# Kernel tuning notes

Measured on AMD Instinct MI355X. Metric: run time of the kernel, lower is better.

Reference implementation:

```python
import jax, jax.numpy as jnp
import numpy as np

N_NODES = 10000
N_EDGES = 160000
MUL = 128            # channel multiplicity of node features
N_ELEM = 10          # node_attrs scalars (num elements)
N_EDGE_FEATS = 8     # radial basis size
W_NUMEL = 4 * MUL    # 4 uvu paths, 128 weights each
AVG_NEIGH = 16.0
INV_SQRT3 = 0.5773502691896258  # CG coefficient for 1o x 1o -> 0e (dot product path)


def setup_inputs() -> dict:
    key = jax.random.key(0)
    ks = jax.random.split(key, 12)
    node_attrs = jax.random.uniform(ks[0], (N_NODES, N_ELEM), dtype=jnp.float32)
    node_feats = jax.random.normal(ks[1], (N_NODES, MUL * 4), dtype=jnp.float32)  # 128x0e + 128x1o flattened
    edge_attrs = jax.random.normal(ks[2], (N_EDGES, 4), dtype=jnp.float32)        # Y0 (1) + Y1 (3)
    edge_feats = jax.random.normal(ks[3], (N_EDGES, N_EDGE_FEATS), dtype=jnp.float32)
    edge_index = jax.random.randint(ks[4], (2, N_EDGES), 0, N_NODES, dtype=jnp.int64)
    # learned parameters (xavier-ish scales; e3nn path norms folded into weights)
    W_up0 = jax.random.normal(ks[5], (MUL, MUL), dtype=jnp.float32) / np.sqrt(MUL)
    W_up1 = jax.random.normal(ks[6], (MUL, MUL), dtype=jnp.float32) / np.sqrt(MUL)
    W_tpw = jax.random.normal(ks[7], (N_ELEM, N_EDGE_FEATS, W_NUMEL), dtype=jnp.float32) / np.sqrt(N_ELEM * N_EDGE_FEATS)
    W_lin0 = jax.random.normal(ks[8], (2 * MUL, MUL), dtype=jnp.float32) / np.sqrt(2 * MUL)
    W_lin1 = jax.random.normal(ks[9], (2 * MUL, MUL), dtype=jnp.float32) / np.sqrt(2 * MUL)
    W_sk0 = jax.random.normal(ks[10], (MUL, N_ELEM, MUL), dtype=jnp.float32) / np.sqrt(MUL * N_ELEM)
    W_sk1 = jax.random.normal(ks[11], (MUL, N_ELEM, MUL), dtype=jnp.float32) / np.sqrt(MUL * N_ELEM)
    return dict(node_attrs=node_attrs, node_feats=node_feats, edge_attrs=edge_attrs,
                edge_feats=edge_feats, edge_index=edge_index,
                W_up0=W_up0, W_up1=W_up1, W_tpw=W_tpw,
                W_lin0=W_lin0, W_lin1=W_lin1, W_sk0=W_sk0, W_sk1=W_sk1)


def reference(node_attrs, node_feats, edge_attrs, edge_feats, edge_index,
              W_up0, W_up1, W_tpw, W_lin0, W_lin1, W_sk0, W_sk1):
    N = node_feats.shape[0]
    sender, receiver = edge_index[0], edge_index[1]
    x0 = node_feats[:, :MUL]                       # [N,128] scalars (0e)
    x1 = node_feats[:, MUL:].reshape(N, MUL, 3)    # [N,128,3] vectors (1o)

    # skip_tp: FullyConnectedTensorProduct(node_feats, node_attrs -> 128x0e+128x1o)
    sc0 = jnp.einsum('nu,na,uak->nk', x0, node_attrs, W_sk0)        # [N,128]
    sc1 = jnp.einsum('num,na,uak->nkm', x1, node_attrs, W_sk1)      # [N,128,3]

    # linear_up: per-l linear
    h0 = x0 @ W_up0                                   # [N,128]
    h1 = jnp.einsum('num,uk->nkm', x1, W_up1)         # [N,128,3]

    # per-edge TP weights: einsum('be,ba,aek->bk')
    tpw = jnp.einsum('be,ba,aek->bk', edge_feats, node_attrs[sender], W_tpw)  # [E,512]
    w1, w2, w3, w4 = tpw[:, :MUL], tpw[:, MUL:2*MUL], tpw[:, 2*MUL:3*MUL], tpw[:, 3*MUL:]

    Y0 = edge_attrs[:, 0]       # [E]
    Y1 = edge_attrs[:, 1:4]     # [E,3]
    hs0 = h0[sender]            # [E,128] gather
    hs1 = h1[sender]            # [E,128,3]

    # conv_tp (uvu, external per-edge weights), 4 CG paths:
    m0a = w1 * hs0 * Y0[:, None]                                       # 0e x 0e -> 0e
    m1a = (w2 * hs0)[:, :, None] * Y1[:, None, :]                      # 0e x 1o -> 1o
    m1b = hs1 * (w3 * Y0[:, None])[:, :, None]                         # 1o x 0e -> 1o
    m0b = w4 * (INV_SQRT3 * jnp.einsum('eum,em->eu', hs1, Y1))         # 1o x 1o -> 0e
    m0 = jnp.concatenate([m0a, m0b], axis=1)    # [E,256]  irreps_mid 0e block
    m1 = jnp.concatenate([m1a, m1b], axis=1)    # [E,256,3] irreps_mid 1o block

    # scatter_sum over receiver
    msg0 = jax.ops.segment_sum(m0, receiver, num_segments=N)   # [N,256]
    msg1 = jax.ops.segment_sum(m1, receiver, num_segments=N)   # [N,256,3]

    # linear (irreps_mid -> 128x0e+128x1o) / avg_num_neighbors + skip
    out0 = (msg0 @ W_lin0) / AVG_NEIGH + sc0                        # [N,128]
    out1 = jnp.einsum('num,uk->nkm', msg1, W_lin1) / AVG_NEIGH + sc1  # [N,128,3]
    return jnp.concatenate([out0, out1.reshape(N, MUL * 3)], axis=1)  # [N,512]
```

## Files before the change

### kernel.cpp

```cpp
#include <hip/hip_runtime.h>

#define NN 10000
#define NE 160000
#define NBK0 157
#define NBK1 469

constexpr float INV_AVG = 1.0f / 16.0f;
constexpr float INV_SQRT3F = 0.5773502691896258f;

typedef __attribute__((ext_vector_type(8))) short short8v;
typedef __attribute__((ext_vector_type(8))) unsigned short ushort8v;
typedef __attribute__((ext_vector_type(4))) float float4v;

#define OF_UP0 0
#define OF_UP1 16384
#define OF_SK0 32768
#define OF_SK1 196608
#define OF_LN0 360448
#define OF_LN1 393216
#define WPK_TOT 425984
#define WTP_TOT 49152

__device__ __forceinline__ unsigned short f2bf(float f) {
    unsigned int u = __float_as_uint(f);
    return (unsigned short)((u + 0x7FFFu + ((u >> 16) & 1u)) >> 16);
}
__device__ __forceinline__ float bf2f(unsigned short h) {
    return __uint_as_float(((unsigned int)h) << 16);
}

__global__ __launch_bounds__(256) void prep_w_kernel(
    const float* __restrict__ W_up0, const float* __restrict__ W_up1,
    const float* __restrict__ W_sk0, const float* __restrict__ W_sk1,
    const float* __restrict__ W_lin0, const float* __restrict__ W_lin1,
    unsigned short* __restrict__ wpk)
{
    const int g = blockIdx.x * 256 + threadIdx.x;
    if (g >= WPK_TOT / 8) return;
    const float* src; int local, base;
    if (g < 2048)       { src = W_up0;  local = g;         base = OF_UP0; }
    else if (g < 4096)  { src = W_up1;  local = g - 2048;  base = OF_UP1; }
    else if (g < 24576) { src = W_sk0;  local = g - 4096;  base = OF_SK0; }
    else if (g < 45056) { src = W_sk1;  local = g - 24576; base = OF_SK1; }
    else if (g < 49152) { src = W_lin0; local = g - 45056; base = OF_LN0; }
    else                { src = W_lin1; local = g - 49152; base = OF_LN1; }
    const int k8 = local >> 7, n = local & 127;
    ushort8v v;
    #pragma unroll
    for (int j = 0; j < 8; ++j)
        v[j] = f2bf(src[(size_t)(k8 * 8 + j) * 128 + n]);
    *(ushort8v*)(wpk + (size_t)base + (size_t)local * 8) = v;
}

__global__ __launch_bounds__(256) void prep_wt_kernel(
    const float* __restrict__ W_tpw, unsigned short* __restrict__ wtp)
{
    const int g = blockIdx.x * 256 + threadIdx.x;
    if (g >= 6144) return;
    const int k8 = g >> 9, col = g & 511;
    ushort8v v;
    #pragma unroll
    for (int j = 0; j < 8; ++j) {
        const int k = k8 * 8 + j;
        v[j] = (k < 80) ? f2bf(W_tpw[(size_t)k * 512 + col]) : (unsigned short)0;
    }
    *(ushort8v*)(wtp + (size_t)g * 8) = v;
}

__global__ __launch_bounds__(256, 2) void node_mfma_kernel(
    const float* __restrict__ node_attrs,
    const float* __restrict__ node_feats,
    const unsigned short* __restrict__ wpk,
    float* __restrict__ hbuf,
    float* __restrict__ out)
{
    __shared__ __align__(16) unsigned short habuf[1024][8];
    __shared__ __align__(16) unsigned short abuf[512][8];
    __shared__ __align__(16) unsigned short bbuf[1024][8];

    const int t = threadIdx.x;
    const int bid = blockIdx.x;
    const bool m1 = (bid >= NBK0);
    const int r0 = m1 ? (bid - NBK0) * 64 : bid * 64;
    const int RTOT = m1 ? 30000 : 10000;

    const unsigned short* __restrict__ wup = wpk + (m1 ? OF_UP1 : OF_UP0);
    const unsigned short* __restrict__ wsk = wpk + (m1 ? OF_SK1 : OF_SK0);

    const int rg_ = t >> 2, pg_ = t & 3;
    const int rr_g = min(r0 + rg_, RTOT - 1);
    int n_g, m_g;
    if (!m1) { n_g = rr_g; m_g = 0; }
    else     { n_g = rr_g / 3; m_g = rr_g - n_g * 3; }
    const int wq = rg_ >> 4, rlq = rg_ & 15;

    float atr[10];
    #pragma unroll
    for (int a = 0; a < 10; ++a) atr[a] = node_attrs[n_g * 10 + a];

    #pragma unroll
    for (int q = 0; q < 4; ++q) {
        const int sl = pg_ * 4 + q, ss = sl >> 2, kb = sl & 3;
        const int k0 = ss * 32 + kb * 8;
        ushort8v v;
        if (!m1) {
            const float4 xa_ = *(const float4*)(node_feats + (size_t)n_g * 512 + k0);
            const float4 xb_ = *(const float4*)(node_feats + (size_t)n_g * 512 + k0 + 4);
            v[0] = f2bf(xa_.x); v[1] = f2bf(xa_.y); v[2] = f2bf(xa_.z); v[3] = f2bf(xa_.w);
            v[4] = f2bf(xb_.x); v[5] = f2bf(xb_.y); v[6] = f2bf(xb_.z); v[7] = f2bf(xb_.w);
        } else {
            #pragma unroll
            for (int j = 0; j < 8; ++j)
                v[j] = f2bf(node_feats[(size_t)n_g * 512 + 128 + (k0 + j) * 3 + m_g]);
        }
        *(ushort8v*)&habuf[((ss * 4 + wq) * 4 + kb) * 16 + rlq][0] = v;
    }
    __syncthreads();

    const int w = t >> 6, lane = t & 63;
    const int rl = lane & 15, kq = lane >> 4;

    {
        float4v hacc[8];
        #pragma unroll
        for (int nt = 0; nt < 8; ++nt) hacc[nt] = (float4v){0.f, 0.f, 0.f, 0.f};

        #pragma unroll
        for (int ss = 0; ss < 4; ++ss) {
            const short8v af = *(const short8v*)&habuf[((ss * 4 + w) * 4 + kq) * 16 + rl][0];
            #pragma unroll
            for (int nt = 0; nt < 8; ++nt) {
                const short8v bf = *(const short8v*)(wup +
                    ((size_t)((ss * 4 + kq) * 128 + nt * 16 + rl)) * 8);
                hacc[nt] = __builtin_amdgcn_mfma_f32_16x16x32_bf16(af, bf, hacc[nt], 0, 0, 0);
            }
        }
        #pragma unroll
        for (int nt = 0; nt < 8; ++nt)
            #pragma unroll
            for (int v2 = 0; v2 < 4; ++v2) {
                const int rr = r0 + w * 16 + kq * 4 + v2;
                if (rr < RTOT) {
                    const int col = nt * 16 + rl;
                    if (!m1) hbuf[(size_t)rr * 512 + col] = hacc[nt][v2];
                    else {
                        const int n = rr / 3, m = rr - n * 3;
                        hbuf[(size_t)n * 512 + 128 + m * 128 + col] = hacc[nt][v2];
                    }
                }
            }
    }

    float4v sacc[8];
    #pragma unroll
    for (int nt = 0; nt < 8; ++nt) sacc[nt] = (float4v){0.f, 0.f, 0.f, 0.f};

    for (int ks = 0; ks < 20; ++ks) {
        __syncthreads();

        #pragma unroll
        for (int s2 = 0; s2 < 2; ++s2) {
            const int sl = pg_ * 2 + s2, ss = sl >> 2, kb = sl & 3;
            const int k0 = ks * 64 + ss * 32 + kb * 8;
            ushort8v v;
            #pragma unroll
            for (int j = 0; j < 8; ++j) {
                const int k = k0 + j;
                const int u = k / 10, a = k - u * 10;
                const unsigned short xh =
                    habuf[(((u >> 5) * 4 + wq) * 4 + ((u >> 3) & 3)) * 16 + rlq][u & 7];
                v[j] = f2bf(bf2f(xh) * atr[a]);
            }
            *(ushort8v*)&abuf[((ss * 4 + wq) * 4 + kb) * 16 + rlq][0] = v;
        }

        #pragma unroll
        for (int i = 0; i < 4; ++i) {
            const int s = i * 256 + t;
            const int ssb = s >> 9, ntb = (s >> 6) & 7, kbb = (s >> 4) & 3, nlb = s & 15;
            const int k8 = ks * 8 + ssb * 4 + kbb;
            const int n = ntb * 16 + nlb;
            *(ushort8v*)&bbuf[s][0] =
                *(const ushort8v*)(wsk + ((size_t)(k8 * 128 + n)) * 8);
        }
        __syncthreads();

        #pragma unroll
        for (int ss = 0; ss < 2; ++ss) {
            const short8v af = *(const short8v*)&abuf[((ss * 4 + w) * 4 + kq) * 16 + rl][0];
            #pragma unroll
            for (int nt = 0; nt < 8; ++nt) {
                const short8v bf = *(const short8v*)&bbuf[((ss * 8 + nt) * 4 + kq) * 16 + rl][0];
                sacc[nt] = __builtin_amdgcn_mfma_f32_16x16x32_bf16(af, bf, sacc[nt], 0, 0, 0);
            }
        }
    }

    #pragma unroll
    for (int nt = 0; nt < 8; ++nt)
        #pragma unroll
        for (int v2 = 0; v2 < 4; ++v2) {
            const int rr = r0 + w * 16 + kq * 4 + v2;
            if (rr < RTOT) {
                const int col = nt * 16 + rl;
                if (!m1) out[(size_t)rr * 512 + col] = sacc[nt][v2];
                else {
                    const int n = rr / 3, m = rr - n * 3;
                    out[(size_t)n * 512 + 128 + col * 3 + m] = sacc[nt][v2];
                }
            }
        }
}

__global__ __launch_bounds__(256) void hist_kernel(
    const int* __restrict__ recv, int* __restrict__ cnt)
{
    const int e = blockIdx.x * 256 + threadIdx.x;
    if (e < NE) atomicAdd(&cnt[recv[e]], 1);
}

__global__ __launch_bounds__(256) void scan_kernel(
    const int* __restrict__ cnt, int* __restrict__ row_start,
    int* __restrict__ head)
{
    __shared__ int part[256];
    const int t = threadIdx.x;
    const int base = t * 40;
    int s = 0;
    if (base < NN)
        for (int b = 0; b < 40; ++b) s += cnt[base + b];
    part[t] = s;
    __syncthreads();
    const int local = s;
    for (int off = 1; off < 256; off <<= 1) {
        const int v = (t >= off) ? part[t - off] : 0;
        __syncthreads();
        part[t] += v;
        __syncthreads();
    }
    const int excl = part[t] - local;
    if (base < NN) {
        int run = excl;
        for (int b = 0; b < 40; ++b) {
            row_start[base + b] = run;
            head[base + b] = run;
            run += cnt[base + b];
        }
    }
    if (t == 0) row_start[NN] = NE;
}

__global__ __launch_bounds__(256) void scatter_kernel(
    const int* __restrict__ recv, int* __restrict__ head,
    int* __restrict__ elist)
{
    const int e = blockIdx.x * 256 + threadIdx.x;
    if (e < NE) {
        const int p = atomicAdd(&head[recv[e]], 1);
        elist[p] = e;
    }
}

__global__ __launch_bounds__(256) void pack2_kernel(
    const float* __restrict__ node_attrs,
    const float* __restrict__ edge_attrs,
    const float* __restrict__ edge_feats,
    const int*  __restrict__ edge_index,
    const int*  __restrict__ elist,
    unsigned short* __restrict__ zpk,
    float* __restrict__ ypk)
{
    const int pos = blockIdx.x * 256 + threadIdx.x;
    if (pos >= NE) return;
    const int e = elist[pos];
    const int snd = edge_index[e];

    float ef[8];
    *(float4*)&ef[0] = *(const float4*)(edge_feats + (size_t)e * 8);
    *(float4*)&ef[4] = *(const float4*)(edge_feats + (size_t)e * 8 + 4);
    float at[10];
    #pragma unroll
    for (int a = 0; a < 10; ++a) at[a] = node_attrs[(size_t)snd * 10 + a];

    #pragma unroll
    for (int k8 = 0; k8 < 12; ++k8) {
        ushort8v v;
        #pragma unroll
        for (int j = 0; j < 8; ++j) {
            const int A = k8 * 8 + j;
            const float z = (A < 80) ? at[A >> 3] * ef[A & 7] : 0.f;
            v[j] = f2bf(z);
        }
        *(ushort8v*)(zpk + ((size_t)k8 * NE + pos) * 8) = v;
    }

    const float4 ea = *(const float4*)(edge_attrs + (size_t)e * 4);
    *(float4*)(ypk + (size_t)pos * 8) = ea;
    *(float4*)(ypk + (size_t)pos * 8 + 4) =
        make_float4(__int_as_float(snd), 0.f, 0.f, 0.f);
}

__global__ __launch_bounds__(256, 2) void gather_mfma_kernel(
    const unsigned short* __restrict__ wtp,
    const float* __restrict__ hbuf,
    const int*  __restrict__ row_start,
    const unsigned short* __restrict__ zpk,
    const float* __restrict__ ypk,
    float* __restrict__ msgbuf)
{
    __shared__ __align__(16) unsigned short zb[384][8];
    __shared__ float yb[32][9];

    const int t = threadIdx.x;
    const int p = blockIdx.x & 1;
    const int ngrp = blockIdx.x >> 1;
    const int w = t >> 6, lane = t & 63;
    const int rl = lane & 15, kq = lane >> 4;

    short8v breg[2][3][2];
    #pragma unroll
    for (int wi = 0; wi < 2; ++wi)
        #pragma unroll
        for (int ks = 0; ks < 3; ++ks)
            #pragma unroll
            for (int ct = 0; ct < 2; ++ct) {
                const int col = p * 256 + wi * 128 + w * 32 + ct * 16 + rl;
                breg[wi][ks][ct] = *(const short8v*)(wtp +
                    ((size_t)((ks * 4 + kq) * 512 + col)) * 8);
            }

    for (int nn = 0; nn < 4; ++nn) {
        const int node = ngrp * 4 + nn;
        const int rowst = row_start[node];
        const int deg = row_start[node + 1] - rowst;

        float nacc[2][4];
        #pragma unroll
        for (int ct = 0; ct < 2; ++ct)
            #pragma unroll
            for (int j = 0; j < 4; ++j) nacc[ct][j] = 0.f;

        for (int ce = 0; ce < deg; ce += 32) {
            const int cl = min(32, deg - ce);
            __syncthreads();

            {
                const int s = t;
                const int rl2 = s & 15, kq2 = (s >> 4) & 3;
                const int rowt2 = (s >> 6) & 1, ks2 = s >> 7;
                const int e = rowt2 * 16 + rl2;
                const int k8 = ks2 * 4 + kq2;
                ushort8v v = {0, 0, 0, 0, 0, 0, 0, 0};
                if (e < cl)
                    v = *(const ushort8v*)(zpk + ((size_t)k8 * NE + rowst + ce + e) * 8);
                *(ushort8v*)&zb[s][0] = v;
            }
            {
                const int s = 256 + t;
                if (s < 384) {
                    const int rl2 = s & 15, kq2 = (s >> 4) & 3;
                    const int rowt2 = (s >> 6) & 1, ks2 = s >> 7;
                    const int e = rowt2 * 16 + rl2;
                    const int k8 = ks2 * 4 + kq2;
                    ushort8v v = {0, 0, 0, 0, 0, 0, 0, 0};
                    if (e < cl)
                        v = *(const ushort8v*)(zpk + ((size_t)k8 * NE + rowst + ce + e) * 8);
                    *(ushort8v*)&zb[s][0] = v;
                }
            }
            if (t < 64) {
                const int row = t >> 1, half = t & 1;
                float4 v = make_float4(0.f, 0.f, 0.f, 0.f);
                if (row < cl)
                    v = *(const float4*)(ypk + (size_t)(rowst + ce + row) * 8 + half * 4);
                yb[row][half * 4 + 0] = v.x;
                yb[row][half * 4 + 1] = v.y;
                yb[row][half * 4 + 2] = v.z;
                yb[row][half * 4 + 3] = v.w;
            }
            __syncthreads();

            if (p == 0) {
                #pragma unroll
                for (int rt = 0; rt < 2; ++rt) {
                    if (rt == 1 && cl <= 16) continue;
                    float h0v[4][2];
                    #pragma unroll
                    for (int v = 0; v < 4; ++v) {
                        const int e = rt * 16 + kq * 4 + v;
                        const int snd = __float_as_int(yb[e][4]);
                        const float* hrow = hbuf + (size_t)snd * 512;
                        #pragma unroll
                        for (int ct = 0; ct < 2; ++ct)
                            h0v[v][ct] = hrow[w * 32 + ct * 16 + rl];
                    }
                    float4v acc[2][2];
                    #pragma unroll
                    for (int wi = 0; wi < 2; ++wi)
                        #pragma unroll
                        for (int ct = 0; ct < 2; ++ct)
                            acc[wi][ct] = (float4v){0.f, 0.f, 0.f, 0.f};
                    #pragma unroll
                    for (int ks = 0; ks < 3; ++ks) {
                        const short8v af =
                            *(const short8v*)&zb[ks * 128 + rt * 64 + lane][0];
                        #pragma unroll
                        for (int wi = 0; wi < 2; ++wi)
                            #pragma unroll
                            for (int ct = 0; ct < 2; ++ct)
                                acc[wi][ct] = __builtin_amdgcn_mfma_f32_16x16x32_bf16(
                                    af, breg[wi][ks][ct], acc[wi][ct], 0, 0, 0);
                    }
                    #pragma unroll
                    for (int v = 0; v < 4; ++v) {
                        const int e = rt * 16 + kq * 4 + v;
                        const float Y0  = yb[e][0];
                        const float Y10 = yb[e][1];
                        const float Y11 = yb[e][2];
                        const float Y12 = yb[e][3];
                        #pragma unroll
                        for (int ct = 0; ct < 2; ++ct) {
                            const float tA = acc[0][ct][v];
                            const float tB = acc[1][ct][v];
                            const float h0 = h0v[v][ct];
                            nacc[ct][0] = fmaf(tA * Y0, h0, nacc[ct][0]);
                            const float tm = tB * h0;
                            nacc[ct][1] = fmaf(tm, Y10, nacc[ct][1]);
                            nacc[ct][2] = fmaf(tm, Y11, nacc[ct][2]);
                            nacc[ct][3] = fmaf(tm, Y12, nacc[ct][3]);
                        }
                    }
                }
            } else {
                #pragma unroll
                for (int rt = 0; rt < 2; ++rt) {
                    if (rt == 1 && cl <= 16) continue;
                    float hA[4][2], hB[4][2], hC[4][2];
                    #pragma unroll
                    for (int v = 0; v < 4; ++v) {
                        const int e = rt * 16 + kq * 4 + v;
                        const int snd = __float_as_int(yb[e][4]);
                        const float* hrow = hbuf + (size_t)snd * 512;
                        #pragma unroll
                        for (int ct = 0; ct < 2; ++ct) {
                            const int c = w * 32 + ct * 16 + rl;
                            hA[v][ct] = hrow[128 + c];
                            hB[v][ct] = hrow[256 + c];
                            hC[v][ct] = hrow[384 + c];
                        }
                    }
                    float4v acc[2][2];
                    #pragma unroll
                    for (int wi = 0; wi < 2; ++wi)
                        #pragma unroll
                        for (int ct = 0; ct < 2; ++ct)
                            acc[wi][ct] = (float4v){0.f, 0.f, 0.f, 0.f};
                    #pragma unroll
                    for (int ks = 0; ks < 3; ++ks) {
                        const short8v af =
                            *(const short8v*)&zb[ks * 128 + rt * 64 + lane][0];
                        #pragma unroll
                        for (int wi = 0; wi < 2; ++wi)
                            #pragma unroll
                            for (int ct = 0; ct < 2; ++ct)
                                acc[wi][ct] = __builtin_amdgcn_mfma_f32_16x16x32_bf16(
                                    af, breg[wi][ks][ct], acc[wi][ct], 0, 0, 0);
                    }
                    #pragma unroll
                    for (int v = 0; v < 4; ++v) {
                        const int e = rt * 16 + kq * 4 + v;
                        const float Y0  = yb[e][0];
                        const float Y10 = yb[e][1];
                        const float Y11 = yb[e][2];
                        const float Y12 = yb[e][3];
                        #pragma unroll
                        for (int ct = 0; ct < 2; ++ct) {
                            const float tA = acc[0][ct][v];
                            const float tB = acc[1][ct][v];
                            const float t2 = tA * Y0;
                            nacc[ct][1] = fmaf(t2, hA[v][ct], nacc[ct][1]);
                            nacc[ct][2] = fmaf(t2, hB[v][ct], nacc[ct][2]);
                            nacc[ct][3] = fmaf(t2, hC[v][ct], nacc[ct][3]);
                            float d = hA[v][ct] * Y10;
                            d = fmaf(hB[v][ct], Y11, d);
                            d = fmaf(hC[v][ct], Y12, d);
                            nacc[ct][0] = fmaf(tB * INV_SQRT3F, d, nacc[ct][0]);
                        }
                    }
                }
            }
        }

        float red[2][4];
        #pragma unroll
        for (int ct = 0; ct < 2; ++ct)
            #pragma unroll
            for (int j = 0; j < 4; ++j) {
                float v = nacc[ct][j];
                v += __shfl_xor(v, 16, 64);
                v += __shfl_xor(v, 32, 64);
                red[ct][j] = v;
            }
        if (kq == 0) {
            float* mrow = msgbuf + (size_t)node * 1024;
            #pragma unroll
            for (int ct = 0; ct < 2; ++ct) {
                const int c = w * 32 + ct * 16 + rl;
                if (p == 0) {
                    mrow[c]       = red[ct][0];
                    mrow[256 + c] = red[ct][1];
                    mrow[512 + c] = red[ct][2];
                    mrow[768 + c] = red[ct][3];
                } else {
                    mrow[128 + c] = red[ct][0];
                    mrow[384 + c] = red[ct][1];
                    mrow[640 + c] = red[ct][2];
                    mrow[896 + c] = red[ct][3];
                }
            }
        }
    }
}

__global__ __launch_bounds__(256, 2) void out_mfma_kernel(
    const float* __restrict__ msgbuf,
    const unsigned short* __restrict__ wpk,
    float* __restrict__ out)
{
    __shared__ __align__(16) unsigned short habuf[2048][8];

    const int t = threadIdx.x;
    const int n0 = blockIdx.x * 16;

    const int rg_ = t >> 2, pg_ = t & 3;
    const int wq = rg_ >> 4, rlq = rg_ & 15;
    const float* src = msgbuf + (size_t)(n0 + rlq) * 1024 + wq * 256;

    #pragma unroll
    for (int q = 0; q < 8; ++q) {
        const int sl = pg_ * 8 + q, ss = sl >> 2, kb = sl & 3;
        const int k0 = ss * 32 + kb * 8;
        const float4 xa = *(const float4*)(src + k0);
        const float4 xb = *(const float4*)(src + k0 + 4);
        ushort8v v;
        v[0] = f2bf(xa.x); v[1] = f2bf(xa.y); v[2] = f2bf(xa.z); v[3] = f2bf(xa.w);
        v[4] = f2bf(xb.x); v[5] = f2bf(xb.y); v[6] = f2bf(xb.z); v[7] = f2bf(xb.w);
        *(ushort8v*)&habuf[((ss * 4 + wq) * 4 + kb) * 16 + rlq][0] = v;
    }
    __syncthreads();

    const int w = t >> 6, lane = t & 63;
    const int rl = lane & 15, kq = lane >> 4;
    const unsigned short* __restrict__ wl = wpk + ((w == 0) ? OF_LN0 : OF_LN1);

    float4v acc[8];
    #pragma unroll
    for (int nt = 0; nt < 8; ++nt) acc[nt] = (float4v){0.f, 0.f, 0.f, 0.f};

    #pragma unroll
    for (int ss = 0; ss < 8; ++ss) {
        const short8v af = *(const short8v*)&habuf[((ss * 4 + w) * 4 + kq) * 16 + rl][0];
        #pragma unroll
        for (int nt = 0; nt < 8; ++nt) {
            const short8v bf = *(const short8v*)(wl +
                ((size_t)((ss * 4 + kq) * 128 + nt * 16 + rl)) * 8);
            acc[nt] = __builtin_amdgcn_mfma_f32_16x16x32_bf16(af, bf, acc[nt], 0, 0, 0);
        }
    }

    #pragma unroll
    for (int nt = 0; nt < 8; ++nt)
        #pragma unroll
        for (int v2 = 0; v2 < 4; ++v2) {
            const int n = n0 + kq * 4 + v2;
            const int col = nt * 16 + rl;
            if (w == 0) {
                out[(size_t)n * 512 + col] += acc[nt][v2] * INV_AVG;
            } else {
                const int m = w - 1;
                out[(size_t)n * 512 + 128 + col * 3 + m] += acc[nt][v2] * INV_AVG;
            }
        }
}

extern "C" void kernel_launch(void* const* d_in, const int* in_sizes, int n_in,
                              void* d_out, int out_size, void* d_ws, size_t ws_size,
                              hipStream_t stream) {
    const float* node_attrs = (const float*)d_in[0];
    const float* node_feats = (const float*)d_in[1];
    const float* edge_attrs = (const float*)d_in[2];
    const float* edge_feats = (const float*)d_in[3];
    const int*   edge_index = (const int*)d_in[4];
    const float* W_up0  = (const float*)d_in[5];
    const float* W_up1  = (const float*)d_in[6];
    const float* W_tpw  = (const float*)d_in[7];
    const float* W_lin0 = (const float*)d_in[8];
    const float* W_lin1 = (const float*)d_in[9];
    const float* W_sk0  = (const float*)d_in[10];
    const float* W_sk1  = (const float*)d_in[11];
    float* out = (float*)d_out;

    float* hbuf   = (float*)d_ws;
    float* msgbuf = hbuf + (size_t)NN * 512;
    float* ypk    = msgbuf + (size_t)NN * 1024;
    unsigned short* zpk = (unsigned short*)(ypk + (size_t)NE * 8);
    unsigned short* wpk = zpk + (size_t)12 * NE * 8;
    unsigned short* wtp = wpk + WPK_TOT;
    int* cnt       = (int*)(wtp + WTP_TOT);
    int* row_start = cnt + NN;
    int* head      = row_start + NN + 1;
    int* elist     = head + NN;

    const int* recv = edge_index + NE;

    hipMemsetAsync(cnt, 0, NN * sizeof(int), stream);
    hist_kernel<<<(NE + 255) / 256, 256, 0, stream>>>(recv, cnt);
    scan_kernel<<<1, 256, 0, stream>>>(cnt, row_start, head);
    scatter_kernel<<<(NE + 255) / 256, 256, 0, stream>>>(recv, head, elist);
    pack2_kernel<<<(NE + 255) / 256, 256, 0, stream>>>(
        node_attrs, edge_attrs, edge_feats, edge_index, elist, zpk, ypk);
    prep_w_kernel<<<(WPK_TOT / 8 + 255) / 256, 256, 0, stream>>>(
        W_up0, W_up1, W_sk0, W_sk1, W_lin0, W_lin1, wpk);
    prep_wt_kernel<<<24, 256, 0, stream>>>(W_tpw, wtp);

    node_mfma_kernel<<<NBK0 + NBK1, 256, 0, stream>>>(node_attrs, node_feats,
                                                      wpk, hbuf, out);
    gather_mfma_kernel<<<5000, 256, 0, stream>>>(wtp, hbuf, row_start,
                                                 zpk, ypk, msgbuf);
    out_mfma_kernel<<<NN / 16, 256, 0, stream>>>(msgbuf, wpk, out);
}
```

Measured before the change: 245.3 us.

## Reorder skip weights by element and double-buffer skip GEMM B tiles

The skip-connection weight packing is permuted so the K index runs element-major (a*128+u). Each 8-wide A fragment then shares one node_attr scalar and can be built directly in registers from habuf, which removes the abuf staging through LDS and the per-element divide/modulo. The weight tile for the next k-step is prefetched into registers and written to a second LDS buffer, cutting the barriers per iteration from two to one and overlapping global loads with MFMA work. In exchange, LDS use per block rises (double-buffered bbuf plus an atrow table) and register pressure goes up.

Measured after the change: 208.2 us. 1.18x faster.

```diff
diff --git a/kernel.cpp b/kernel.cpp
--- a/kernel.cpp
+++ b/kernel.cpp
@@ -37,18 +37,27 @@
 {
     const int g = blockIdx.x * 256 + threadIdx.x;
     if (g >= WPK_TOT / 8) return;
-    const float* src; int local, base;
+    const float* src; int local, base; bool sk = false;
     if (g < 2048)       { src = W_up0;  local = g;         base = OF_UP0; }
     else if (g < 4096)  { src = W_up1;  local = g - 2048;  base = OF_UP1; }
-    else if (g < 24576) { src = W_sk0;  local = g - 4096;  base = OF_SK0; }
-    else if (g < 45056) { src = W_sk1;  local = g - 24576; base = OF_SK1; }
+    else if (g < 24576) { src = W_sk0;  local = g - 4096;  base = OF_SK0; sk = true; }
+    else if (g < 45056) { src = W_sk1;  local = g - 24576; base = OF_SK1; sk = true; }
     else if (g < 49152) { src = W_lin0; local = g - 45056; base = OF_LN0; }
     else                { src = W_lin1; local = g - 49152; base = OF_LN1; }
     const int k8 = local >> 7, n = local & 127;
     ushort8v v;
     #pragma unroll
-    for (int j = 0; j < 8; ++j)
-        v[j] = f2bf(src[(size_t)(k8 * 8 + j) * 128 + n]);
+    for (int j = 0; j < 8; ++j) {
+        const int k = k8 * 8 + j;
+        int row;
+        if (sk) {
+            const int a = k >> 7, u = k & 127;
+            row = u * 10 + a;
+        } else {
+            row = k;
+        }
+        v[j] = f2bf(src[(size_t)row * 128 + n]);
+    }
     *(ushort8v*)(wpk + (size_t)base + (size_t)local * 8) = v;
 }
 
@@ -75,8 +84,8 @@
     float* __restrict__ out)
 {
     __shared__ __align__(16) unsigned short habuf[1024][8];
-    __shared__ __align__(16) unsigned short abuf[512][8];
-    __shared__ __align__(16) unsigned short bbuf[1024][8];
+    __shared__ __align__(16) unsigned short bbuf[2][1024][8];
+    __shared__ float atrow[64][10];
 
     const int t = threadIdx.x;
     const int bid = blockIdx.x;
@@ -93,10 +102,6 @@
     if (!m1) { n_g = rr_g; m_g = 0; }
     else     { n_g = rr_g / 3; m_g = rr_g - n_g * 3; }
     const int wq = rg_ >> 4, rlq = rg_ & 15;
-
-    float atr[10];
-    #pragma unroll
-    for (int a = 0; a < 10; ++a) atr[a] = node_attrs[n_g * 10 + a];
 
     #pragma unroll
     for (int q = 0; q < 4; ++q) {
@@ -115,6 +120,12 @@
         }
         *(ushort8v*)&habuf[((ss * 4 + wq) * 4 + kb) * 16 + rlq][0] = v;
     }
+    for (int i = t; i < 640; i += 256) {
+        const int r = i / 10, a = i - r * 10;
+        const int rr = min(r0 + r, RTOT - 1);
+        const int n = m1 ? (rr / 3) : rr;
+        atrow[r][a] = node_attrs[n * 10 + a];
+    }
     __syncthreads();
 
     const int w = t >> 6, lane = t & 63;
@@ -155,45 +166,63 @@
     #pragma unroll
     for (int nt = 0; nt < 8; ++nt) sacc[nt] = (float4v){0.f, 0.f, 0.f, 0.f};
 
+    #pragma unroll
+    for (int i = 0; i < 4; ++i) {
+        const int s = i * 256 + t;
+        const int ssb = s >> 9, ntb = (s >> 6) & 7, kbb = (s >> 4) & 3, nlb = s & 15;
+        const int k8 = ssb * 4 + kbb;
+        const int n = ntb * 16 + nlb;
+        *(ushort8v*)&bbuf[0][s][0] =
+            *(const ushort8v*)(wsk + ((size_t)(k8 * 128 + n)) * 8);
+    }
+    __syncthreads();
+
+    int cur = 0;
     for (int ks = 0; ks < 20; ++ks) {
+        ushort8v tmp[4];
+        if (ks < 19) {
+            #pragma unroll
+            for (int i = 0; i < 4; ++i) {
+                const int s = i * 256 + t;
+                const int ssb = s >> 9, ntb = (s >> 6) & 7, kbb = (s >> 4) & 3, nlb = s & 15;
+                const int k8 = (ks + 1) * 8 + ssb * 4 + kbb;
+                const int n = ntb * 16 + nlb;
+                tmp[i] = *(const ushort8v*)(wsk + ((size_t)(k8 * 128 + n)) * 8);
+            }
+        }
+
+        short8v af[2];
+        #pragma unroll
+        for (int ss = 0; ss < 2; ++ss) {
+            const int kp = ks * 64 + ss * 32 + kq * 8;
+            const int a = kp >> 7, u0 = kp & 127;
+            const ushort8v xh = *(const ushort8v*)&habuf[
+                (((u0 >> 5) * 4 + w) * 4 + ((u0 >> 3) & 3)) * 16 + rl][0];
+            const float av = atrow[w * 16 + rl][a];
+            ushort8v vv;
+            #pragma unroll
+            for (int j = 0; j < 8; ++j) vv[j] = f2bf(bf2f(xh[j]) * av);
+            af[ss] = (short8v)vv;
+        }
+
+        #pragma unroll
+        for (int ss = 0; ss < 2; ++ss)
+            #pragma unroll
+            for (int nt = 0; nt < 8; ++nt) {
+                const short8v bf =
+                    *(const short8v*)&bbuf[cur][((ss * 8 + nt) * 4 + kq) * 16 + rl][0];
+                sacc[nt] = __builtin_amdgcn_mfma_f32_16x16x32_bf16(af[ss], bf, sacc[nt], 0, 0, 0);
+            }
+
+        if (ks < 19) {
+            #pragma unroll
+            for (int i = 0; i < 4; ++i) {
+                const int s = i * 256 + t;
+                *(ushort8v*)&bbuf[cur ^ 1][s][0] = tmp[i];
+            }
+        }
         __syncthreads();
-
-        #pragma unroll
-        for (int s2 = 0; s2 < 2; ++s2) {
-            const int sl = pg_ * 2 + s2, ss = sl >> 2, kb = sl & 3;
-            const int k0 = ks * 64 + ss * 32 + kb * 8;
-            ushort8v v;
-            #pragma unroll
-            for (int j = 0; j < 8; ++j) {
-                const int k = k0 + j;
-                const int u = k / 10, a = k - u * 10;
-                const unsigned short xh =
-                    habuf[(((u >> 5) * 4 + wq) * 4 + ((u >> 3) & 3)) * 16 + rlq][u & 7];
-                v[j] = f2bf(bf2f(xh) * atr[a]);
-            }
-            *(ushort8v*)&abuf[((ss * 4 + wq) * 4 + kb) * 16 + rlq][0] = v;
-        }
-
-        #pragma unroll
-        for (int i = 0; i < 4; ++i) {
-            const int s = i * 256 + t;
-            const int ssb = s >> 9, ntb = (s >> 6) & 7, kbb = (s >> 4) & 3, nlb = s & 15;
-            const int k8 = ks * 8 + ssb * 4 + kbb;
-            const int n = ntb * 16 + nlb;
-            *(ushort8v*)&bbuf[s][0] =
-                *(const ushort8v*)(wsk + ((size_t)(k8 * 128 + n)) * 8);
-        }
-        __syncthreads();
-
-        #pragma unroll
-        for (int ss = 0; ss < 2; ++ss) {
-            const short8v af = *(const short8v*)&abuf[((ss * 4 + w) * 4 + kq) * 16 + rl][0];
-            #pragma unroll
-            for (int nt = 0; nt < 8; ++nt) {
-                const short8v bf = *(const short8v*)&bbuf[((ss * 8 + nt) * 4 + kq) * 16 + rl][0];
-                sacc[nt] = __builtin_amdgcn_mfma_f32_16x16x32_bf16(af, bf, sacc[nt], 0, 0, 0);
-            }
-        }
+        cur ^= 1;
     }
 
     #pragma unroll
```
